# Kernel tuning notes

Hardware: AMD Instinct MI355X
Metric: run time of the kernel (lower is better)

The kernel has to match this reference:

```python
import jax, jax.numpy as jnp
import numpy as np

N_USERS = 100000
N_ITEMS = 50000
N_NODES = N_USERS + N_ITEMS
DIM = 128
N_HOPS = 3
N_EDGES = 4800000


def setup_inputs() -> dict:
    key = jax.random.key(0)
    ks = jax.random.split(key, 7)
    user_embed = jax.random.normal(ks[0], (N_USERS, DIM), dtype=jnp.float32)
    item_embed = jax.random.normal(ks[1], (N_ITEMS, DIM), dtype=jnp.float32)
    # user_t / item_t are sigmoid(log(deg+e)) priors in (0,1)
    user_t = jax.random.uniform(ks[2], (N_USERS, 1), dtype=jnp.float32)
    item_t = jax.random.uniform(ks[3], (N_ITEMS, 1), dtype=jnp.float32)
    adj_vals = jax.random.uniform(ks[4], (N_EDGES,), dtype=jnp.float32)
    adj_rows = jax.random.randint(ks[5], (N_EDGES,), 0, N_NODES, dtype=jnp.int32)
    adj_cols = jax.random.randint(ks[6], (N_EDGES,), 0, N_NODES, dtype=jnp.int32)
    return {
        "user_embed": user_embed,
        "item_embed": item_embed,
        "user_t": user_t,
        "item_t": item_t,
        "adj_vals": adj_vals,
        "adj_rows": adj_rows,
        "adj_cols": adj_cols,
    }


def _spmm(vals, rows, cols, x):
    # y[r] += vals * x[cols]  -- sparse (N,N) @ dense (N,D)
    msgs = vals[:, None] * x[cols]
    return jax.ops.segment_sum(msgs, rows, num_segments=N_NODES)


def reference(user_embed, item_embed, user_t, item_t, adj_vals, adj_rows, adj_cols):
    # eval-mode GraphConv.forward (no edge/mess dropout)
    agg = jnp.concatenate([user_embed, item_embed], axis=0)  # [N, D]
    ego = jnp.concatenate([user_t * user_embed, item_t * item_embed], axis=0)
    embs = [ego]
    decay_u = 1.0 - user_t
    decay_i = 1.0 - item_t
    pow_u = jnp.ones_like(user_t)
    pow_i = jnp.ones_like(item_t)
    for _ in range(N_HOPS):
        side = _spmm(adj_vals, adj_rows, adj_cols, agg)  # [N, D]
        u_side, i_side = side[:N_USERS], side[N_USERS:]
        pow_u = pow_u * decay_u
        pow_i = pow_i * decay_i
        u_k = u_side * (user_t * pow_u)
        i_k = i_side * (item_t * pow_i)
        embs.append(jnp.concatenate([u_k, i_k], axis=0))
        agg = side
    embs = jnp.stack(embs, axis=1)  # [N, n_hops+1, D]
    return embs[:N_USERS], embs[N_USERS:]
```

## Files before the change

kernel.cpp:

```cpp
#include <hip/hip_runtime.h>

#define NU 100000
#define NI 50000
#define NN 150000
#define DIM 128
#define NHOPS 3
#define STR ((NHOPS + 1) * DIM)


__global__ void hist_kernel(const int* __restrict__ rows, int* deg, int E) {
  int i = blockIdx.x * blockDim.x + threadIdx.x;
  int stride = gridDim.x * blockDim.x;
  for (; i < E; i += stride) atomicAdd(&deg[rows[i]], 1);
}

__global__ void scan_kernel(int* deg_cursor, int* row_start, int n, int total) {
  __shared__ int sums[1024];
  int t = threadIdx.x;
  int chunk = (n + 1023) >> 10;
  int beg = t * chunk;
  int end = beg + chunk; if (end > n) end = n;
  int s = 0;
  for (int i = beg; i < end; ++i) s += deg_cursor[i];
  sums[t] = s;
  __syncthreads();
  for (int off = 1; off < 1024; off <<= 1) {
    int v = (t >= off) ? sums[t - off] : 0;
    __syncthreads();
    sums[t] += v;
    __syncthreads();
  }
  int run = sums[t] - s;
  for (int i = beg; i < end; ++i) {
    int d = deg_cursor[i];
    row_start[i] = run;
    deg_cursor[i] = run;
    run += d;
  }
  if (t == 0) row_start[n] = total;
}

__global__ void scatter_kernel(const int* __restrict__ rows, const int* __restrict__ cols,
                               const float* __restrict__ vals, int* cursor,
                               int* __restrict__ csr_col, float* __restrict__ csr_val, int E) {
  int i = blockIdx.x * blockDim.x + threadIdx.x;
  int stride = gridDim.x * blockDim.x;
  for (; i < E; i += stride) {
    int r = rows[i];
    int p = atomicAdd(&cursor[r], 1);
    csr_col[p] = cols[i];
    csr_val[p] = vals[i];
  }
}


__global__ void copy_embed_kernel(const float* __restrict__ ue, const float* __restrict__ ie,
                                  float* __restrict__ out) {
  int idx = blockIdx.x * blockDim.x + threadIdx.x;
  if (idx >= NN * (DIM / 4)) return;
  int node = idx >> 5;
  int d4 = idx & 31;
  const float4* src = (node < NU)
      ? ((const float4*)(ue + (size_t)node * DIM) + d4)
      : ((const float4*)(ie + (size_t)(node - NU) * DIM) + d4);
  ((float4*)(out + (size_t)node * STR))[d4] = *src;
}

__global__ void spmm_kernel(const int* __restrict__ row_start, const int* __restrict__ csr_col,
                            const float* __restrict__ csr_val, const float* base_in,
                            float* base_out, int kin_off, int kout_off) {
  int wave = (blockIdx.x * blockDim.x + threadIdx.x) >> 6;
  if (wave >= NN) return;
  int lane = threadIdx.x & 63;
  int s = row_start[wave];
  int e = row_start[wave + 1];
  float ax = 0.f, ay = 0.f;
  const float* src_base = base_in + kin_off + lane * 2;
  int p = s;
  for (; p + 8 <= e; p += 8) {
    int c = csr_col[p + (lane & 7)];
    float v = csr_val[p + (lane & 7)];
#pragma unroll
    for (int j = 0; j < 8; ++j) {
      int cc = __shfl(c, j);
      float vv = __shfl(v, j);
      float2 x = *(const float2*)(src_base + (size_t)cc * STR);
      ax += vv * x.x;
      ay += vv * x.y;
    }
  }
  for (; p < e; ++p) {
    int cc = csr_col[p];
    float vv = csr_val[p];
    float2 x = *(const float2*)(src_base + (size_t)cc * STR);
    ax += vv * x.x;
    ay += vv * x.y;
  }
  float2 o; o.x = ax; o.y = ay;
  *(float2*)(base_out + (size_t)wave * STR + kout_off + lane * 2) = o;
}

__global__ void spmm_atomic_kernel(const int* __restrict__ rows, const int* __restrict__ cols,
                                   const float* __restrict__ vals, const float* base_in,
                                   float* base_out, int kin_off, int kout_off, int E) {
  int wave = (blockIdx.x * blockDim.x + threadIdx.x) >> 6;
  if (wave >= E) return;
  int lane = threadIdx.x & 63;
  int r = rows[wave], c = cols[wave];
  float v = vals[wave];
  float2 x = *(const float2*)(base_in + (size_t)c * STR + kin_off + lane * 2);
  float* dst = base_out + (size_t)r * STR + kout_off + lane * 2;
  atomicAdd(dst, v * x.x);
  atomicAdd(dst + 1, v * x.y);
}

__global__ void epilogue_kernel(const float* __restrict__ ut, const float* __restrict__ it,
                                float* __restrict__ out) {
  int idx = blockIdx.x * blockDim.x + threadIdx.x;
  if (idx >= NN * (STR / 4)) return;
  int node = idx >> 7;
  int rem = idx & 127;
  int k = rem >> 5;
  float t = (node < NU) ? ut[node] : it[node - NU];
  float dcy = 1.f - t;
  float sc = t;
  for (int j = 0; j < k; ++j) sc *= dcy;
  float4* p = (float4*)out + idx;
  float4 x = *p;
  x.x *= sc; x.y *= sc; x.z *= sc; x.w *= sc;
  *p = x;
}


extern "C" void kernel_launch(void* const* d_in, const int* in_sizes, int n_in,
                              void* d_out, int out_size, void* d_ws, size_t ws_size,
                              hipStream_t stream) {
  const float* ue = (const float*)d_in[0];
  const float* ie = (const float*)d_in[1];
  const float* ut = (const float*)d_in[2];
  const float* it = (const float*)d_in[3];
  const float* vals = (const float*)d_in[4];
  const int* rows = (const int*)d_in[5];
  const int* cols = (const int*)d_in[6];
  float* out = (float*)d_out;
  const int E = in_sizes[4];

  size_t off = 0;
  auto alloc = [&](size_t bytes) {
    void* p = (char*)d_ws + off;
    off += (bytes + 255) & ~(size_t)255;
    return p;
  };
  int* cursor = (int*)alloc((size_t)NN * 4);
  int* rstart = (int*)alloc(((size_t)NN + 1) * 4);
  int* csr_col = (int*)alloc((size_t)E * 4);
  float* csr_val = (float*)alloc((size_t)E * 4);
  bool use_csr = (off <= ws_size);

  const int n4_embed = NN * (DIM / 4);

  if (use_csr) {
    copy_embed_kernel<<<(n4_embed + 255) / 256, 256, 0, stream>>>(ue, ie, out);
    hipMemsetAsync(cursor, 0, (size_t)NN * 4, stream);
    hist_kernel<<<2048, 256, 0, stream>>>(rows, cursor, E);
    scan_kernel<<<1, 1024, 0, stream>>>(cursor, rstart, NN, E);
    scatter_kernel<<<2048, 256, 0, stream>>>(rows, cols, vals, cursor, csr_col, csr_val, E);
    for (int h = 1; h <= NHOPS; ++h) {
      spmm_kernel<<<(NN + 3) / 4, 256, 0, stream>>>(rstart, csr_col, csr_val, out, out,
                                                    (h - 1) * DIM, h * DIM);
    }
  } else {
    hipMemsetAsync(out, 0, (size_t)out_size * 4, stream);
    copy_embed_kernel<<<(n4_embed + 255) / 256, 256, 0, stream>>>(ue, ie, out);
    for (int h = 1; h <= NHOPS; ++h) {
      long threads = (long)E * 64;
      spmm_atomic_kernel<<<(threads + 255) / 256, 256, 0, stream>>>(rows, cols, vals, out, out,
                                                                    (h - 1) * DIM, h * DIM, E);
    }
  }

  const int n4_out = NN * (STR / 4);
  epilogue_kernel<<<(n4_out + 255) / 256, 256, 0, stream>>>(ut, it, out);
}
```

Before: 2.218 ms.

## Parallelize CSR scan, pack edges, fuse hop scaling into SpMM with compact buffers

Replaces the single-block serial prefix scan with a three-kernel block scan. Column indices and values are packed into one int2 array so each edge is a single load. Each hop now reads from and writes to compact raw buffers with a 128-float stride, which improves gather locality over the interleaved 512-float-stride output. The per-hop decay scaling is fused into the SpMM store, which removes the separate epilogue pass. The cost is extra workspace for two raw buffers and an extra write of raw hop results, and the atomic fallback path is dropped.

```diff
diff --git a/kernel.cpp b/kernel.cpp
--- a/kernel.cpp
+++ b/kernel.cpp
@@ -14,48 +14,91 @@
   for (; i < E; i += stride) atomicAdd(&deg[rows[i]], 1);
 }
 
-__global__ void scan_kernel(int* deg_cursor, int* row_start, int n, int total) {
-  __shared__ int sums[1024];
-  int t = threadIdx.x;
-  int chunk = (n + 1023) >> 10;
-  int beg = t * chunk;
-  int end = beg + chunk; if (end > n) end = n;
+__global__ void scan_k1(const int* __restrict__ deg, int* bsum, int n) {
+  __shared__ int red[256];
+  int b = blockIdx.x, t = threadIdx.x;
+  int base = b * 2048 + t * 8;
   int s = 0;
-  for (int i = beg; i < end; ++i) s += deg_cursor[i];
-  sums[t] = s;
+#pragma unroll
+  for (int j = 0; j < 8; ++j) { int i = base + j; if (i < n) s += deg[i]; }
+  red[t] = s;
   __syncthreads();
-  for (int off = 1; off < 1024; off <<= 1) {
-    int v = (t >= off) ? sums[t - off] : 0;
+  for (int off = 128; off > 0; off >>= 1) {
+    if (t < off) red[t] += red[t + off];
     __syncthreads();
-    sums[t] += v;
+  }
+  if (t == 0) bsum[b] = red[0];
+}
+
+__global__ void scan_k2(int* bsum, int nb) {
+  if (threadIdx.x == 0) {
+    int run = 0;
+    for (int i = 0; i < nb; ++i) { int v = bsum[i]; bsum[i] = run; run += v; }
+  }
+}
+
+__global__ void scan_k3(const int* __restrict__ deg, const int* __restrict__ bsum,
+                        int* __restrict__ rstart, int* __restrict__ cursor, int n, int E) {
+  __shared__ int red[256];
+  int b = blockIdx.x, t = threadIdx.x;
+  int base = b * 2048 + t * 8;
+  int loc[8];
+  int s = 0;
+#pragma unroll
+  for (int j = 0; j < 8; ++j) {
+    int i = base + j;
+    int d = (i < n) ? deg[i] : 0;
+    loc[j] = s; s += d;
+  }
+  red[t] = s;
+  __syncthreads();
+  for (int off = 1; off < 256; off <<= 1) {
+    int v = (t >= off) ? red[t - off] : 0;
     __syncthreads();
-  }
-  int run = sums[t] - s;
-  for (int i = beg; i < end; ++i) {
-    int d = deg_cursor[i];
-    row_start[i] = run;
-    deg_cursor[i] = run;
-    run += d;
-  }
-  if (t == 0) row_start[n] = total;
+    red[t] += v;
+    __syncthreads();
+  }
+  int toff = bsum[b] + red[t] - s;
+#pragma unroll
+  for (int j = 0; j < 8; ++j) {
+    int i = base + j;
+    if (i < n) { int v = toff + loc[j]; rstart[i] = v; cursor[i] = v; }
+  }
+  if (b == 0 && t == 0) rstart[n] = E;
 }
 
 __global__ void scatter_kernel(const int* __restrict__ rows, const int* __restrict__ cols,
                                const float* __restrict__ vals, int* cursor,
-                               int* __restrict__ csr_col, float* __restrict__ csr_val, int E) {
+                               int2* __restrict__ csr, int E) {
   int i = blockIdx.x * blockDim.x + threadIdx.x;
   int stride = gridDim.x * blockDim.x;
   for (; i < E; i += stride) {
     int r = rows[i];
     int p = atomicAdd(&cursor[r], 1);
-    csr_col[p] = cols[i];
-    csr_val[p] = vals[i];
-  }
-}
-
-
-__global__ void copy_embed_kernel(const float* __restrict__ ue, const float* __restrict__ ie,
-                                  float* __restrict__ out) {
+    int2 e; e.x = cols[i]; e.y = __float_as_int(vals[i]);
+    csr[p] = e;
+  }
+}
+
+
+__global__ void copy_embed_fused(const float* __restrict__ ue, const float* __restrict__ ie,
+                                 const float* __restrict__ ut, const float* __restrict__ it,
+                                 float* __restrict__ rawA, float* __restrict__ out) {
+  int idx = blockIdx.x * blockDim.x + threadIdx.x;
+  if (idx >= NN * (DIM / 4)) return;
+  int node = idx >> 5;
+  int d4 = idx & 31;
+  float t;
+  float4 x;
+  if (node < NU) { t = ut[node]; x = ((const float4*)(ue + (size_t)node * DIM))[d4]; }
+  else { t = it[node - NU]; x = ((const float4*)(ie + (size_t)(node - NU) * DIM))[d4]; }
+  ((float4*)(rawA + (size_t)node * DIM))[d4] = x;
+  float4 y; y.x = x.x * t; y.y = x.y * t; y.z = x.z * t; y.w = x.w * t;
+  ((float4*)(out + (size_t)node * STR))[d4] = y;
+}
+
+__global__ void copy_embed_raw(const float* __restrict__ ue, const float* __restrict__ ie,
+                               float* __restrict__ out) {
   int idx = blockIdx.x * blockDim.x + threadIdx.x;
   if (idx >= NN * (DIM / 4)) return;
   int node = idx >> 5;
@@ -66,66 +109,63 @@
   ((float4*)(out + (size_t)node * STR))[d4] = *src;
 }
 
-__global__ void spmm_kernel(const int* __restrict__ row_start, const int* __restrict__ csr_col,
-                            const float* __restrict__ csr_val, const float* base_in,
-                            float* base_out, int kin_off, int kout_off) {
+__global__ void spmm_kernel(const int* __restrict__ row_start, const int2* __restrict__ csr,
+                            const float* __restrict__ src, int src_str,
+                            float* raw_out, int raw_str,
+                            float* scaled_out, int scaled_str,
+                            const float* __restrict__ ut, const float* __restrict__ it, int hop) {
   int wave = (blockIdx.x * blockDim.x + threadIdx.x) >> 6;
   if (wave >= NN) return;
   int lane = threadIdx.x & 63;
   int s = row_start[wave];
   int e = row_start[wave + 1];
   float ax = 0.f, ay = 0.f;
-  const float* src_base = base_in + kin_off + lane * 2;
+  const float* src_base = src + lane * 2;
   int p = s;
   for (; p + 8 <= e; p += 8) {
-    int c = csr_col[p + (lane & 7)];
-    float v = csr_val[p + (lane & 7)];
+    int2 ed = csr[p + (lane & 7)];
 #pragma unroll
     for (int j = 0; j < 8; ++j) {
-      int cc = __shfl(c, j);
-      float vv = __shfl(v, j);
-      float2 x = *(const float2*)(src_base + (size_t)cc * STR);
+      int cc = __shfl(ed.x, j);
+      float vv = __int_as_float(__shfl(ed.y, j));
+      float2 x = *(const float2*)(src_base + (size_t)cc * src_str);
       ax += vv * x.x;
       ay += vv * x.y;
     }
   }
   for (; p < e; ++p) {
-    int cc = csr_col[p];
-    float vv = csr_val[p];
-    float2 x = *(const float2*)(src_base + (size_t)cc * STR);
+    int2 ed = csr[p];
+    float2 x = *(const float2*)(src_base + (size_t)ed.x * src_str);
+    float vv = __int_as_float(ed.y);
     ax += vv * x.x;
     ay += vv * x.y;
   }
-  float2 o; o.x = ax; o.y = ay;
-  *(float2*)(base_out + (size_t)wave * STR + kout_off + lane * 2) = o;
-}
-
-__global__ void spmm_atomic_kernel(const int* __restrict__ rows, const int* __restrict__ cols,
-                                   const float* __restrict__ vals, const float* base_in,
-                                   float* base_out, int kin_off, int kout_off, int E) {
-  int wave = (blockIdx.x * blockDim.x + threadIdx.x) >> 6;
-  if (wave >= E) return;
-  int lane = threadIdx.x & 63;
-  int r = rows[wave], c = cols[wave];
-  float v = vals[wave];
-  float2 x = *(const float2*)(base_in + (size_t)c * STR + kin_off + lane * 2);
-  float* dst = base_out + (size_t)r * STR + kout_off + lane * 2;
-  atomicAdd(dst, v * x.x);
-  atomicAdd(dst + 1, v * x.y);
+  if (raw_out) {
+    float2 o; o.x = ax; o.y = ay;
+    *(float2*)(raw_out + (size_t)wave * raw_str + lane * 2) = o;
+  }
+  if (scaled_out) {
+    float t = (wave < NU) ? ut[wave] : it[wave - NU];
+    float sc = t;
+    for (int j = 0; j < hop; ++j) sc *= (1.f - t);
+    float2 o; o.x = ax * sc; o.y = ay * sc;
+    *(float2*)(scaled_out + (size_t)wave * scaled_str + lane * 2) = o;
+  }
 }
 
 __global__ void epilogue_kernel(const float* __restrict__ ut, const float* __restrict__ it,
                                 float* __restrict__ out) {
   int idx = blockIdx.x * blockDim.x + threadIdx.x;
-  if (idx >= NN * (STR / 4)) return;
-  int node = idx >> 7;
-  int rem = idx & 127;
+  if (idx >= NN * 96) return;
+  int node = idx / 96;
+  int rem = idx - node * 96;
   int k = rem >> 5;
+  int d4 = rem & 31;
   float t = (node < NU) ? ut[node] : it[node - NU];
   float dcy = 1.f - t;
   float sc = t;
   for (int j = 0; j < k; ++j) sc *= dcy;
-  float4* p = (float4*)out + idx;
+  float4* p = (float4*)(out + (size_t)node * STR + k * DIM) + d4;
   float4 x = *p;
   x.x *= sc; x.y *= sc; x.z *= sc; x.w *= sc;
   *p = x;
@@ -151,34 +191,49 @@
     off += (bytes + 255) & ~(size_t)255;
     return p;
   };
+  int* deg = (int*)alloc((size_t)NN * 4);
   int* cursor = (int*)alloc((size_t)NN * 4);
   int* rstart = (int*)alloc(((size_t)NN + 1) * 4);
-  int* csr_col = (int*)alloc((size_t)E * 4);
-  float* csr_val = (float*)alloc((size_t)E * 4);
-  bool use_csr = (off <= ws_size);
+  int* bsum = (int*)alloc(1024 * 4);
+  int2* csr = (int2*)alloc((size_t)E * 8);
+  size_t csr_end = off;
+  float* rawA = (float*)alloc((size_t)NN * DIM * 4);
+  float* rawB = (float*)alloc((size_t)NN * DIM * 4);
+  bool use_csr = (csr_end <= ws_size);
+  bool use_compact = (off <= ws_size);
 
   const int n4_embed = NN * (DIM / 4);
+  const int nb_scan = (NN + 2047) / 2048;
+  const int spmm_blocks = (NN + 3) / 4;
 
   if (use_csr) {
-    copy_embed_kernel<<<(n4_embed + 255) / 256, 256, 0, stream>>>(ue, ie, out);
-    hipMemsetAsync(cursor, 0, (size_t)NN * 4, stream);
-    hist_kernel<<<2048, 256, 0, stream>>>(rows, cursor, E);
-    scan_kernel<<<1, 1024, 0, stream>>>(cursor, rstart, NN, E);
-    scatter_kernel<<<2048, 256, 0, stream>>>(rows, cols, vals, cursor, csr_col, csr_val, E);
-    for (int h = 1; h <= NHOPS; ++h) {
-      spmm_kernel<<<(NN + 3) / 4, 256, 0, stream>>>(rstart, csr_col, csr_val, out, out,
-                                                    (h - 1) * DIM, h * DIM);
+    hipMemsetAsync(deg, 0, (size_t)NN * 4, stream);
+    hist_kernel<<<2048, 256, 0, stream>>>(rows, deg, E);
+    scan_k1<<<nb_scan, 256, 0, stream>>>(deg, bsum, NN);
+    scan_k2<<<1, 64, 0, stream>>>(bsum, nb_scan);
+    scan_k3<<<nb_scan, 256, 0, stream>>>(deg, bsum, rstart, cursor, NN, E);
+    scatter_kernel<<<2048, 256, 0, stream>>>(rows, cols, vals, cursor, csr, E);
+
+    if (use_compact) {
+      copy_embed_fused<<<(n4_embed + 255) / 256, 256, 0, stream>>>(ue, ie, ut, it, rawA, out);
+      float* rin = rawA;
+      float* rout = rawB;
+      for (int h = 1; h <= NHOPS; ++h) {
+        float* raw_dst = (h < NHOPS) ? rout : nullptr;
+        spmm_kernel<<<spmm_blocks, 256, 0, stream>>>(rstart, csr, rin, DIM,
+                                                     raw_dst, DIM,
+                                                     out + h * DIM, STR, ut, it, h);
+        float* tmp = rin; rin = rout; rout = tmp;
+      }
+    } else {
+      copy_embed_raw<<<(n4_embed + 255) / 256, 256, 0, stream>>>(ue, ie, out);
+      for (int h = 1; h <= NHOPS; ++h) {
+        float* raw_dst = (h < NHOPS) ? (out + h * DIM) : nullptr;
+        float* sc_dst = (h == NHOPS) ? (out + h * DIM) : nullptr;
+        spmm_kernel<<<spmm_blocks, 256, 0, stream>>>(rstart, csr, out + (h - 1) * DIM, STR,
+                                                     raw_dst, STR, sc_dst, STR, ut, it, h);
+      }
+      epilogue_kernel<<<(NN * 96 + 255) / 256, 256, 0, stream>>>(ut, it, out);
     }
-  } else {
-    hipMemsetAsync(out, 0, (size_t)out_size * 4, stream);
-    copy_embed_kernel<<<(n4_embed + 255) / 256, 256, 0, stream>>>(ue, ie, out);
-    for (int h = 1; h <= NHOPS; ++h) {
-      long threads = (long)E * 64;
-      spmm_atomic_kernel<<<(threads + 255) / 256, 256, 0, stream>>>(rows, cols, vals, out, out,
-                                                                    (h - 1) * DIM, h * DIM, E);
-    }
-  }
-
-  const int n4_out = NN * (STR / 4);
-  epilogue_kernel<<<(n4_out + 255) / 256, 256, 0, stream>>>(ut, it, out);
-}
+  }
+}
```

Result: faster. 1.936 ms (-12.7%).
